# Optimization experiments

Measured on AMD Instinct MI355X. Metric: run time of the kernel, lower is better.

## Reference

```python
import jax, jax.numpy as jnp
import numpy as np

NUM_HEADS = 16
VALUE_SIZE = 64
MODEL_SIZE = 1024
BATCH = 4
SEQ = 1024


def setup_inputs() -> dict:
    key = jax.random.key(0)
    ks = jax.random.split(key, 5)
    scale = 1.0 / np.sqrt(MODEL_SIZE)
    x = jax.random.normal(ks[0], (BATCH, SEQ, MODEL_SIZE), dtype=jnp.float32)
    w_q = jax.random.normal(ks[1], (MODEL_SIZE, NUM_HEADS * VALUE_SIZE), dtype=jnp.float32) * scale
    w_kv = jax.random.normal(ks[2], (MODEL_SIZE, NUM_HEADS * VALUE_SIZE), dtype=jnp.float32) * scale
    w_o = jax.random.normal(ks[3], (NUM_HEADS * VALUE_SIZE, MODEL_SIZE), dtype=jnp.float32) * scale
    # original init is Constant(0.0); use small random values for a non-trivial test
    k_weights = jax.random.normal(ks[4], (1, NUM_HEADS, 1, VALUE_SIZE), dtype=jnp.float32) * 0.02
    return {"x": x, "w_q": w_q, "w_kv": w_kv, "w_o": w_o, "k_weights": k_weights}


def reference(x, w_q, w_kv, w_o, k_weights):
    b, L, d = x.shape
    h, v = NUM_HEADS, VALUE_SIZE
    # projections (no bias); q scaled by 1/sqrt(model_size)
    q = (x @ w_q) * (1.0 / jnp.sqrt(jnp.asarray(d, x.dtype)))
    q = q.reshape(b, L, h, v).transpose(0, 2, 1, 3)    # b h l v
    kv = (x @ w_kv).reshape(b, L, h, v).transpose(0, 2, 1, 3)  # b h l v
    # learned per-head key scaling on the shared k=v tensor
    k = kv * (1.0 + k_weights)
    logits = jnp.einsum('bhik,bhjk->bhij', q, k)       # b h L L
    mask = jnp.tril(jnp.ones((L, L), dtype=bool))
    logits = jnp.where(mask, logits, jnp.asarray(-1e6, logits.dtype))
    a = jax.nn.softmax(logits, axis=-1)
    y = jnp.einsum('bhij,bhjv->bhiv', a, kv)           # attend over shared kv
    y = y.transpose(0, 2, 1, 3).reshape(b, L, h * v)
    return y @ w_o
```

## Files before the change

kernel.cpp:

```cpp
#include <hip/hip_runtime.h>
#include <hip/hip_bf16.h>
#include <stdint.h>

#define BATCH 4
#define SEQ   1024
#define DMODEL 1024
#define NH    16
#define DV    64

typedef short bf8 __attribute__((ext_vector_type(8)));
typedef float f4  __attribute__((ext_vector_type(4)));

static __device__ __forceinline__ short f2bf(float f) {
    union { float f; uint32_t u; } a; a.f = f;
    uint32_t r = a.u + 0x7FFF + ((a.u >> 16) & 1);
    return (short)(r >> 16);
}

static __device__ __forceinline__ f4 mfma16(bf8 a, bf8 b, f4 c) {
    return __builtin_amdgcn_mfma_f32_16x16x32_bf16(a, b, c, 0, 0, 0);
}

static __device__ __forceinline__ void gload16(const short* g, short* l) {
    __builtin_amdgcn_global_load_lds((const __attribute__((address_space(1))) void*)g,
                                     (__attribute__((address_space(3))) void*)l,
                                     16, 0, 0);
}


__global__ void cvt_x_kernel(const float* __restrict__ x, short* __restrict__ xb) {
    int i = blockIdx.x * blockDim.x + threadIdx.x;
    float4 v = ((const float4*)x)[i];
    short4 o;
    o.x = f2bf(v.x); o.y = f2bf(v.y); o.z = f2bf(v.z); o.w = f2bf(v.w);
    ((short4*)xb)[i] = o;
}

__global__ void transpose_w_kernel(const float* __restrict__ wq, const float* __restrict__ wkv,
                                   const float* __restrict__ wo,
                                   short* __restrict__ wqkvt, short* __restrict__ wot) {
    __shared__ float tile[32][33];
    int z = blockIdx.z;
    const float* w = (z == 0) ? wq : (z == 1) ? wkv : wo;
    short* wt = (z == 0) ? wqkvt : (z == 1) ? (wqkvt + (1u << 20)) : wot;
    int bx = blockIdx.x, by = blockIdx.y;
    int tx = threadIdx.x, ty = threadIdx.y;
    #pragma unroll
    for (int i = 0; i < 4; i++)
        tile[ty + i * 8][tx] = w[(size_t)(by * 32 + ty + i * 8) * 1024 + bx * 32 + tx];
    __syncthreads();
    #pragma unroll
    for (int i = 0; i < 4; i++)
        wt[(size_t)(bx * 32 + ty + i * 8) * 1024 + by * 32 + tx] = f2bf(tile[tx][ty + i * 8]);
}


__global__ __launch_bounds__(256) void gemm_proj_kernel(
    const short* __restrict__ A, const short* __restrict__ Bt,
    const float* __restrict__ kw,
    short* __restrict__ q_out, short* __restrict__ kv_out, short* __restrict__ kvT_out)
{
    __shared__ short SM[2 * 128 * 64];
    short* As = SM;
    short* Bs = SM + 128 * 64;
    const int K = DMODEL;

    int tid = threadIdx.x;
    int wave = tid >> 6, lane = tid & 63;
    int quad = lane >> 4, l16 = lane & 15;
    int m0 = blockIdx.y * 128;
    int n0 = blockIdx.x * 128;
    int wm = (wave >> 1) * 64;
    int wn = (wave & 1) * 64;
    int sw = l16 & 7;

    f4 acc[4][4] = {};

    for (int k0 = 0; k0 < K; k0 += 64) {
        __syncthreads();
        #pragma unroll
        for (int c = 0; c < 4; c++) {
            int flat = c * 256 + tid;
            int row = flat >> 3;
            int seg = (flat & 7) ^ (row & 7);
            gload16(A  + (size_t)(m0 + row) * K + k0 + seg * 8, As + flat * 8);
            gload16(Bt + (size_t)(n0 + row) * K + k0 + seg * 8, Bs + flat * 8);
        }
        __syncthreads();

        #pragma unroll
        for (int kk = 0; kk < 2; kk++) {
            bf8 af[4], bfr[4];
            #pragma unroll
            for (int i = 0; i < 4; i++)
                af[i] = *(const bf8*)(As + (wm + i * 16 + l16) * 64 + ((kk * 4 + quad) ^ sw) * 8);
            #pragma unroll
            for (int j = 0; j < 4; j++)
                bfr[j] = *(const bf8*)(Bs + (wn + j * 16 + l16) * 64 + ((kk * 4 + quad) ^ sw) * 8);
            #pragma unroll
            for (int i = 0; i < 4; i++)
                #pragma unroll
                for (int j = 0; j < 4; j++)
                    acc[i][j] = mfma16(af[i], bfr[j], acc[i][j]);
        }
    }

    #pragma unroll
    for (int i = 0; i < 4; i++) {
        #pragma unroll
        for (int j = 0; j < 4; j++) {
            int n = n0 + wn + j * 16 + l16;
            int mb = m0 + wm + i * 16 + quad * 4;
            float v0 = acc[i][j][0], v1 = acc[i][j][1], v2 = acc[i][j][2], v3 = acc[i][j][3];
            if (n < 1024) {
                float kws = 0.03125f * (1.0f + kw[n]);
                q_out[(size_t)(mb + 0) * 1024 + n] = f2bf(v0 * kws);
                q_out[(size_t)(mb + 1) * 1024 + n] = f2bf(v1 * kws);
                q_out[(size_t)(mb + 2) * 1024 + n] = f2bf(v2 * kws);
                q_out[(size_t)(mb + 3) * 1024 + n] = f2bf(v3 * kws);
            } else {
                int n2 = n - 1024;
                kv_out[(size_t)(mb + 0) * 1024 + n2] = f2bf(v0);
                kv_out[(size_t)(mb + 1) * 1024 + n2] = f2bf(v1);
                kv_out[(size_t)(mb + 2) * 1024 + n2] = f2bf(v2);
                kv_out[(size_t)(mb + 3) * 1024 + n2] = f2bf(v3);
            }
        }
    }

    if (n0 >= 1024) {
        const int TST = 136;
        short* T = SM;
        int n2base = n0 - 1024;
        int mloc = m0 & 1023;
        int bq = m0 >> 10;
        #pragma unroll
        for (int hn = 0; hn < 2; hn++) {
            __syncthreads();
            if ((wave & 1) == hn) {
                #pragma unroll
                for (int i = 0; i < 4; i++) {
                    #pragma unroll
                    for (int j = 0; j < 4; j++) {
                        int nl = j * 16 + l16;
                        int ml = wm + i * 16 + quad * 4;
                        short4 tv;
                        tv.x = f2bf(acc[i][j][0]); tv.y = f2bf(acc[i][j][1]);
                        tv.z = f2bf(acc[i][j][2]); tv.w = f2bf(acc[i][j][3]);
                        *(short4*)(T + nl * TST + ml) = tv;
                    }
                }
            }
            __syncthreads();
            #pragma unroll
            for (int c = 0; c < 4; c++) {
                int flat = c * 256 + tid;
                int row = flat >> 4;
                int seg = flat & 15;
                bf8 vseg = *(const bf8*)(T + row * TST + seg * 8);
                int n2 = n2base + hn * 64 + row;
                int bh = (bq << 4) + (n2 >> 6);
                *(bf8*)(kvT_out + (size_t)(bh * 64 + (n2 & 63)) * 1024 + mloc + seg * 8) = vseg;
            }
        }
    }
}


__global__ __launch_bounds__(256) void gemm_out_kernel(
    const short* __restrict__ A, const short* __restrict__ Bt,
    float* __restrict__ c_out)
{
    __shared__ short As[64 * 64];
    __shared__ short Bs[128 * 64];
    const int K = DMODEL;

    int tid = threadIdx.x;
    int wave = tid >> 6, lane = tid & 63;
    int quad = lane >> 4, l16 = lane & 15;
    int m0 = blockIdx.y * 64;
    int n0 = blockIdx.x * 128;
    int wm = wave * 16;
    int sw = l16 & 7;

    f4 acc[8] = {};

    for (int k0 = 0; k0 < K; k0 += 64) {
        __syncthreads();
        #pragma unroll
        for (int c = 0; c < 2; c++) {
            int flat = c * 256 + tid;
            int row = flat >> 3;
            int seg = (flat & 7) ^ (row & 7);
            gload16(A + (size_t)(m0 + row) * K + k0 + seg * 8, As + flat * 8);
        }
        #pragma unroll
        for (int c = 0; c < 4; c++) {
            int flat = c * 256 + tid;
            int row = flat >> 3;
            int seg = (flat & 7) ^ (row & 7);
            gload16(Bt + (size_t)(n0 + row) * K + k0 + seg * 8, Bs + flat * 8);
        }
        __syncthreads();

        #pragma unroll
        for (int kk = 0; kk < 2; kk++) {
            bf8 af = *(const bf8*)(As + (wm + l16) * 64 + ((kk * 4 + quad) ^ sw) * 8);
            #pragma unroll
            for (int j = 0; j < 8; j++) {
                bf8 bf_ = *(const bf8*)(Bs + (j * 16 + l16) * 64 + ((kk * 4 + quad) ^ sw) * 8);
                acc[j] = mfma16(af, bf_, acc[j]);
            }
        }
    }

    #pragma unroll
    for (int j = 0; j < 8; j++) {
        int n = n0 + j * 16 + l16;
        int mb = m0 + wm + quad * 4;
        c_out[(size_t)(mb + 0) * 1024 + n] = acc[j][0];
        c_out[(size_t)(mb + 1) * 1024 + n] = acc[j][1];
        c_out[(size_t)(mb + 2) * 1024 + n] = acc[j][2];
        c_out[(size_t)(mb + 3) * 1024 + n] = acc[j][3];
    }
}


#define PLD 72

__global__ __launch_bounds__(256) void attn_kernel(
    const short* __restrict__ qg, const short* __restrict__ kvg,
    const short* __restrict__ kvTg, short* __restrict__ yg)
{
    int bh = blockIdx.y;
    int b = bh >> 4, h = bh & 15;
    int x = blockIdx.x;
    int tid = threadIdx.x;
    int wave = tid >> 6, lane = tid & 63;
    int quad = lane >> 4, l16 = lane & 15;
    int qa0 = x * 64;
    int qb0 = (15 - x) * 64;
    int ntiles = 16 - x;

    __shared__ short Ks[2][64 * 64];
    __shared__ short Vs[2][64 * 64];
    __shared__ short Ps[4][16 * PLD];
    short* myP = &Ps[wave][0];

    const short* qpa = qg + (size_t)(b * 1024 + qa0 + wave * 16 + l16) * 1024 + h * 64;
    const short* qpb = qg + (size_t)(b * 1024 + qb0 + wave * 16 + l16) * 1024 + h * 64;
    bf8 qa_0 = *(const bf8*)(qpa + quad * 8);
    bf8 qa_1 = *(const bf8*)(qpa + 32 + quad * 8);
    bf8 qb_0 = *(const bf8*)(qpb + quad * 8);
    bf8 qb_1 = *(const bf8*)(qpb + 32 + quad * 8);

    bf8 ones;
    #pragma unroll
    for (int j = 0; j < 8; j++) ones[j] = (short)0x3F80;

    f4 oa[4] = {}, ob[4] = {};
    f4 lsa = {}, lsb = {};
    int rowbaseA = qa0 + wave * 16 + quad * 4;
    int rowbaseB = qb0 + wave * 16 + quad * 4;

    auto stage = [&](int jt) {
        short* dstK = &Ks[jt & 1][0];
        short* dstV = &Vs[jt & 1][0];
        int j0 = jt * 64;
        #pragma unroll
        for (int k = 0; k < 2; k++) {
            int flat = k * 256 + tid;
            int row = flat >> 3;
            int lseg = (flat & 7) ^ (row & 7);
            gload16(kvg + (size_t)(b * 1024 + j0 + row) * 1024 + h * 64 + lseg * 8,
                    dstK + flat * 8);
            gload16(kvTg + (size_t)(bh * 64 + row) * 1024 + j0 + lseg * 8,
                    dstV + flat * 8);
        }
    };

    auto proc = [&](bf8 qf0, bf8 qf1, int rowbase, int j0,
                    const short* K, const short* V, f4 (&o)[4], f4& lsum) {
        f4 s[4];
        #pragma unroll
        for (int c = 0; c < 4; c++) {
            int row = c * 16 + l16;
            int swz = row & 7;
            bf8 kb0 = *(const bf8*)(K + row * 64 + (quad ^ swz) * 8);
            bf8 kb1 = *(const bf8*)(K + row * 64 + (((quad + 4) ^ swz)) * 8);
            f4 t = {};
            t = mfma16(qf0, kb0, t);
            t = mfma16(qf1, kb1, t);
            s[c] = t;
        }
        #pragma unroll
        for (int r = 0; r < 4; r++) {
            int qi = rowbase + r;
            float p0 = (j0 + l16      <= qi) ? __expf(s[0][r]) : 0.0f;
            float p1 = (j0 + 16 + l16 <= qi) ? __expf(s[1][r]) : 0.0f;
            float p2 = (j0 + 32 + l16 <= qi) ? __expf(s[2][r]) : 0.0f;
            float p3 = (j0 + 48 + l16 <= qi) ? __expf(s[3][r]) : 0.0f;
            int prow = quad * 4 + r;
            myP[prow * PLD + l16]      = f2bf(p0);
            myP[prow * PLD + 16 + l16] = f2bf(p1);
            myP[prow * PLD + 32 + l16] = f2bf(p2);
            myP[prow * PLD + 48 + l16] = f2bf(p3);
        }
        bf8 pf0 = *(const bf8*)(myP + l16 * PLD + quad * 8);
        bf8 pf1 = *(const bf8*)(myP + l16 * PLD + 32 + quad * 8);
        lsum = mfma16(pf0, ones, lsum);
        lsum = mfma16(pf1, ones, lsum);
        #pragma unroll
        for (int t = 0; t < 4; t++) {
            int vrow = t * 16 + l16;
            int swz = vrow & 7;
            bf8 vb0 = *(const bf8*)(V + vrow * 64 + (quad ^ swz) * 8);
            bf8 vb1 = *(const bf8*)(V + vrow * 64 + (((quad + 4) ^ swz)) * 8);
            o[t] = mfma16(pf0, vb0, o[t]);
            o[t] = mfma16(pf1, vb1, o[t]);
        }
    };

    stage(0);

    for (int jt = 0; jt < ntiles; jt++) {
        __syncthreads();
        if (jt + 1 < ntiles) stage(jt + 1);
        const short* K = &Ks[jt & 1][0];
        const short* V = &Vs[jt & 1][0];
        int j0 = jt * 64;
        proc(qb_0, qb_1, rowbaseB, j0, K, V, ob, lsb);
        if (jt <= x)
            proc(qa_0, qa_1, rowbaseA, j0, K, V, oa, lsa);
    }

    {
        float r0 = 1.0f / lsa[0], r1 = 1.0f / lsa[1], r2 = 1.0f / lsa[2], r3 = 1.0f / lsa[3];
        #pragma unroll
        for (int t = 0; t < 4; t++) {
            size_t base = (size_t)(b * SEQ + rowbaseA) * (NH * DV) + h * DV + t * 16 + l16;
            yg[base]                 = f2bf(oa[t][0] * r0);
            yg[base + 1 * (NH * DV)] = f2bf(oa[t][1] * r1);
            yg[base + 2 * (NH * DV)] = f2bf(oa[t][2] * r2);
            yg[base + 3 * (NH * DV)] = f2bf(oa[t][3] * r3);
        }
    }
    {
        float r0 = 1.0f / lsb[0], r1 = 1.0f / lsb[1], r2 = 1.0f / lsb[2], r3 = 1.0f / lsb[3];
        #pragma unroll
        for (int t = 0; t < 4; t++) {
            size_t base = (size_t)(b * SEQ + rowbaseB) * (NH * DV) + h * DV + t * 16 + l16;
            yg[base]                 = f2bf(ob[t][0] * r0);
            yg[base + 1 * (NH * DV)] = f2bf(ob[t][1] * r1);
            yg[base + 2 * (NH * DV)] = f2bf(ob[t][2] * r2);
            yg[base + 3 * (NH * DV)] = f2bf(ob[t][3] * r3);
        }
    }
}


extern "C" void kernel_launch(void* const* d_in, const int* in_sizes, int n_in,
                              void* d_out, int out_size, void* d_ws, size_t ws_size,
                              hipStream_t stream) {
    const float* x    = (const float*)d_in[0];
    const float* w_q  = (const float*)d_in[1];
    const float* w_kv = (const float*)d_in[2];
    const float* w_o  = (const float*)d_in[3];
    const float* kw   = (const float*)d_in[4];
    float* out = (float*)d_out;

    char* ws = (char*)d_ws;
    short* xb    = (short*)(ws);
    short* wqkvt = (short*)(ws + ( 8u << 20));
    short* wot   = (short*)(ws + (12u << 20));
    short* qp    = (short*)(ws + (14u << 20));
    short* kvb   = (short*)(ws + (22u << 20));
    short* kvT   = (short*)(ws + (30u << 20));
    short* yb    = (short*)(ws + (38u << 20));

    cvt_x_kernel<<<4096, 256, 0, stream>>>(x, xb);
    transpose_w_kernel<<<dim3(32, 32, 3), dim3(32, 8), 0, stream>>>(w_q, w_kv, w_o, wqkvt, wot);

    gemm_proj_kernel<<<dim3(16, 32), 256, 0, stream>>>(
        xb, wqkvt, kw, qp, kvb, kvT);

    attn_kernel<<<dim3(8, BATCH * NH), 256, 0, stream>>>(qp, kvb, kvT, yb);

    gemm_out_kernel<<<dim3(8, 64), 256, 0, stream>>>(yb, wot, out);
}
```

Measured before the change: 159.4 us.

## Halve GEMM K-tiles to 32 and split attention into two-wave blocks

The projection and output GEMMs now stage K in chunks of 32 instead of 64, with a matching 4-segment XOR swizzle. This halves shared memory per block so more blocks can be resident, at the cost of twice as many loop iterations and barriers. The attention kernel now uses 128-thread blocks that each handle half of a query-tile pair, doubling the grid to 16x64 for better CU occupancy. In exchange, each K/V tile is loaded by twice as many blocks, which adds global traffic.

```diff
diff --git a/kernel.cpp b/kernel.cpp
--- a/kernel.cpp
+++ b/kernel.cpp
@@ -60,9 +60,9 @@
     const float* __restrict__ kw,
     short* __restrict__ q_out, short* __restrict__ kv_out, short* __restrict__ kvT_out)
 {
-    __shared__ short SM[2 * 128 * 64];
+    __shared__ short SM[8704];
     short* As = SM;
-    short* Bs = SM + 128 * 64;
+    short* Bs = SM + 4096;
     const int K = DMODEL;
 
     int tid = threadIdx.x;
@@ -72,37 +72,34 @@
     int n0 = blockIdx.x * 128;
     int wm = (wave >> 1) * 64;
     int wn = (wave & 1) * 64;
-    int sw = l16 & 7;
+    int fsw = (l16 >> 1) & 3;
 
     f4 acc[4][4] = {};
 
-    for (int k0 = 0; k0 < K; k0 += 64) {
-        __syncthreads();
-        #pragma unroll
-        for (int c = 0; c < 4; c++) {
+    for (int k0 = 0; k0 < K; k0 += 32) {
+        __syncthreads();
+        #pragma unroll
+        for (int c = 0; c < 2; c++) {
             int flat = c * 256 + tid;
-            int row = flat >> 3;
-            int seg = (flat & 7) ^ (row & 7);
+            int row = flat >> 2;
+            int seg = (flat & 3) ^ ((row >> 1) & 3);
             gload16(A  + (size_t)(m0 + row) * K + k0 + seg * 8, As + flat * 8);
             gload16(Bt + (size_t)(n0 + row) * K + k0 + seg * 8, Bs + flat * 8);
         }
         __syncthreads();
 
-        #pragma unroll
-        for (int kk = 0; kk < 2; kk++) {
-            bf8 af[4], bfr[4];
-            #pragma unroll
-            for (int i = 0; i < 4; i++)
-                af[i] = *(const bf8*)(As + (wm + i * 16 + l16) * 64 + ((kk * 4 + quad) ^ sw) * 8);
+        bf8 af[4], bfr[4];
+        #pragma unroll
+        for (int i = 0; i < 4; i++)
+            af[i] = *(const bf8*)(As + (wm + i * 16 + l16) * 32 + (quad ^ fsw) * 8);
+        #pragma unroll
+        for (int j = 0; j < 4; j++)
+            bfr[j] = *(const bf8*)(Bs + (wn + j * 16 + l16) * 32 + (quad ^ fsw) * 8);
+        #pragma unroll
+        for (int i = 0; i < 4; i++)
             #pragma unroll
             for (int j = 0; j < 4; j++)
-                bfr[j] = *(const bf8*)(Bs + (wn + j * 16 + l16) * 64 + ((kk * 4 + quad) ^ sw) * 8);
-            #pragma unroll
-            for (int i = 0; i < 4; i++)
-                #pragma unroll
-                for (int j = 0; j < 4; j++)
-                    acc[i][j] = mfma16(af[i], bfr[j], acc[i][j]);
-        }
+                acc[i][j] = mfma16(af[i], bfr[j], acc[i][j]);
     }
 
     #pragma unroll
@@ -171,8 +168,8 @@
     const short* __restrict__ A, const short* __restrict__ Bt,
     float* __restrict__ c_out)
 {
-    __shared__ short As[64 * 64];
-    __shared__ short Bs[128 * 64];
+    __shared__ short As[64 * 32];
+    __shared__ short Bs[128 * 32];
     const int K = DMODEL;
 
     int tid = threadIdx.x;
@@ -181,36 +178,32 @@
     int m0 = blockIdx.y * 64;
     int n0 = blockIdx.x * 128;
     int wm = wave * 16;
-    int sw = l16 & 7;
+    int fsw = (l16 >> 1) & 3;
 
     f4 acc[8] = {};
 
-    for (int k0 = 0; k0 < K; k0 += 64) {
-        __syncthreads();
+    for (int k0 = 0; k0 < K; k0 += 32) {
+        __syncthreads();
+        {
+            int flat = tid;
+            int row = flat >> 2;
+            int seg = (flat & 3) ^ ((row >> 1) & 3);
+            gload16(A + (size_t)(m0 + row) * K + k0 + seg * 8, As + flat * 8);
+        }
         #pragma unroll
         for (int c = 0; c < 2; c++) {
             int flat = c * 256 + tid;
-            int row = flat >> 3;
-            int seg = (flat & 7) ^ (row & 7);
-            gload16(A + (size_t)(m0 + row) * K + k0 + seg * 8, As + flat * 8);
-        }
-        #pragma unroll
-        for (int c = 0; c < 4; c++) {
-            int flat = c * 256 + tid;
-            int row = flat >> 3;
-            int seg = (flat & 7) ^ (row & 7);
+            int row = flat >> 2;
+            int seg = (flat & 3) ^ ((row >> 1) & 3);
             gload16(Bt + (size_t)(n0 + row) * K + k0 + seg * 8, Bs + flat * 8);
         }
         __syncthreads();
 
-        #pragma unroll
-        for (int kk = 0; kk < 2; kk++) {
-            bf8 af = *(const bf8*)(As + (wm + l16) * 64 + ((kk * 4 + quad) ^ sw) * 8);
-            #pragma unroll
-            for (int j = 0; j < 8; j++) {
-                bf8 bf_ = *(const bf8*)(Bs + (j * 16 + l16) * 64 + ((kk * 4 + quad) ^ sw) * 8);
-                acc[j] = mfma16(af, bf_, acc[j]);
-            }
+        bf8 af = *(const bf8*)(As + (wm + l16) * 32 + (quad ^ fsw) * 8);
+        #pragma unroll
+        for (int j = 0; j < 8; j++) {
+            bf8 bf_ = *(const bf8*)(Bs + (j * 16 + l16) * 32 + (quad ^ fsw) * 8);
+            acc[j] = mfma16(af, bf_, acc[j]);
         }
     }
 
@@ -228,23 +221,24 @@
 
 #define PLD 72
 
-__global__ __launch_bounds__(256) void attn_kernel(
+__global__ __launch_bounds__(128) void attn_kernel(
     const short* __restrict__ qg, const short* __restrict__ kvg,
     const short* __restrict__ kvTg, short* __restrict__ yg)
 {
     int bh = blockIdx.y;
     int b = bh >> 4, h = bh & 15;
-    int x = blockIdx.x;
+    int x = blockIdx.x >> 1;
+    int half = blockIdx.x & 1;
     int tid = threadIdx.x;
     int wave = tid >> 6, lane = tid & 63;
     int quad = lane >> 4, l16 = lane & 15;
-    int qa0 = x * 64;
-    int qb0 = (15 - x) * 64;
+    int qa0 = x * 64 + half * 32;
+    int qb0 = (15 - x) * 64 + half * 32;
     int ntiles = 16 - x;
 
     __shared__ short Ks[2][64 * 64];
     __shared__ short Vs[2][64 * 64];
-    __shared__ short Ps[4][16 * PLD];
+    __shared__ short Ps[2][16 * PLD];
     short* myP = &Ps[wave][0];
 
     const short* qpa = qg + (size_t)(b * 1024 + qa0 + wave * 16 + l16) * 1024 + h * 64;
@@ -268,8 +262,8 @@
         short* dstV = &Vs[jt & 1][0];
         int j0 = jt * 64;
         #pragma unroll
-        for (int k = 0; k < 2; k++) {
-            int flat = k * 256 + tid;
+        for (int k = 0; k < 4; k++) {
+            int flat = k * 128 + tid;
             int row = flat >> 3;
             int lseg = (flat & 7) ^ (row & 7);
             gload16(kvg + (size_t)(b * 1024 + j0 + row) * 1024 + h * 64 + lseg * 8,
@@ -384,7 +378,7 @@
     gemm_proj_kernel<<<dim3(16, 32), 256, 0, stream>>>(
         xb, wqkvt, kw, qp, kvb, kvT);
 
-    attn_kernel<<<dim3(8, BATCH * NH), 256, 0, stream>>>(qp, kvb, kvT, yb);
+    attn_kernel<<<dim3(16, BATCH * NH), 128, 0, stream>>>(qp, kvb, kvT, yb);
 
     gemm_out_kernel<<<dim3(8, 64), 256, 0, stream>>>(yb, wot, out);
 }
```

Result: slower. 164.5 us (+3.2%).
